# Kernel tuning notes

Hardware: AMD Instinct MI355X
Metric: run time of the kernel (lower is better)

The kernel has to match this reference:

```python
import math
import jax, jax.numpy as jnp
import numpy as np

B, S, D_IN, D_OUT = 8, 4096, 512, 512
CHUNK = 64
MAX_LR = 0.2        # config.max_memory_lr
MIN_DECAY = 0.5     # config.min_memory_decay
MAX_NORM = 30.0     # config.memory_max_norm
NORM_EPS = 1e-5     # config.norm_eps (used in normalize_for_delta)


def setup_inputs() -> dict:
    key = jax.random.key(0)
    ks = jax.random.split(key, 5)
    x = jax.random.normal(ks[0], (B, S, D_IN), dtype=jnp.float32)
    # M_init: xavier_uniform(gain=0.1) ~ small; use small normal
    M_init = jax.random.normal(ks[1], (D_OUT, D_IN), dtype=jnp.float32) * 0.02
    # hyperparam projections (Linear(d_in, 1)); torch init: zero weight, logit bias.
    # Use small random weights so the data-dependent path is exercised.
    eta_w = jax.random.normal(ks[2], (1, D_IN), dtype=jnp.float32) * 0.01
    eta_b = jnp.full((1,), math.log(0.08 / 0.92), dtype=jnp.float32)   # inv_sig(memory_lr_init)
    alpha_w = jax.random.normal(ks[3], (1, D_IN), dtype=jnp.float32) * 0.01
    alpha_b = jnp.full((1,), math.log(0.85 / 0.15), dtype=jnp.float32)  # inv_sig(memory_decay_init)
    gate_w = jax.random.normal(ks[4], (1, D_IN), dtype=jnp.float32) * 0.01
    gate_b = jnp.full((1,), 2.0, dtype=jnp.float32)
    return {"x": x, "M_init": M_init, "eta_w": eta_w, "eta_b": eta_b,
            "alpha_w": alpha_w, "alpha_b": alpha_b, "gate_w": gate_w, "gate_b": gate_b}


def _forward(x, M_init, eta_w, eta_b, alpha_w, alpha_b, gate_w, gate_b):
    n_chunks = S // CHUNK
    # [n_chunks, B, C, d_in] for scan over chunks
    xc = x.reshape(B, n_chunks, CHUNK, D_IN).transpose(1, 0, 2, 3)
    M0 = jnp.broadcast_to(M_init, (B, D_OUT, D_IN))

    def step(M, chunk):  # M: [B, d_out, d_in], chunk: [B, C, d_in]
        # per-chunk hyperparams (training mode: base logits = 0)
        eta_tok = jax.nn.sigmoid(chunk @ eta_w.T + eta_b) * MAX_LR            # [B,C,1]
        alpha_tok = MIN_DECAY + jax.nn.sigmoid(chunk @ alpha_w.T + alpha_b) * (1.0 - MIN_DECAY)
        eta = eta_tok.mean(axis=1, keepdims=True)    # [B,1,1]
        alpha = alpha_tok.mean(axis=1, keepdims=True)
        # retrieval: chunk @ M^T
        outputs = jnp.einsum('bcd,bod->bco', chunk, M)  # [B,C,d_out]
        # normalized keys (F.normalize: x / max(||x||, eps))
        kn = jnp.linalg.norm(chunk, axis=-1, keepdims=True)
        keys = chunk / jnp.maximum(kn, NORM_EPS)
        k_mean = keys.mean(axis=1)        # [B,d_in]
        v_target = outputs.mean(axis=1)   # [B,d_out]
        # delta rule rank-1 update
        Mk = jnp.einsum('bod,bd->bo', M, k_mean)
        error = v_target - Mk
        update = error[:, :, None] * k_mean[:, None, :]  # [B,d_out,d_in]
        # chunk_scale = min(C/chunk_size, 1) = 1 here
        M_new = alpha * M + eta * update
        gate = jax.nn.sigmoid(k_mean @ gate_w.T + gate_b)[:, :, None]  # [B,1,1]
        M_new = gate * M_new + (1.0 - gate) * M
        # frobenius-norm clamp
        M_norm = jnp.sqrt(jnp.sum(M_new * M_new, axis=(-2, -1), keepdims=True))
        scale = jnp.minimum(MAX_NORM / (M_norm + 1e-6), 1.0)
        return M_new * scale, outputs

    M_fin, outs = jax.lax.scan(step, M0, xc)  # outs: [n_chunks,B,C,d_out]
    out = outs.transpose(1, 0, 2, 3).reshape(B, S, D_OUT)
    return out, M_fin


def reference(x, M_init, eta_w, eta_b, alpha_w, alpha_b, gate_w, gate_b):
    return _forward(x, M_init, eta_w, eta_b, alpha_w, alpha_b, gate_w, gate_b)
```

## Files before the change

### kernel.cpp

```cpp
#include <hip/hip_runtime.h>
#include <math.h>

#define DIN  512
#define DOUT 512
#define CHK  64
#define NCH  64
#define NB   8
#define SEQ  4096

typedef short bh8_t __attribute__((ext_vector_type(8)));
typedef float f32x4 __attribute__((ext_vector_type(4)));

__device__ __forceinline__ float sigmoidf_(float z){ return 1.0f/(1.0f+__expf(-z)); }

__device__ __forceinline__ unsigned short f2bf(float f){
  unsigned u = __float_as_uint(f);
  unsigned r = (u + 0x7fffu + ((u>>16)&1u)) >> 16;
  return (unsigned short)r;
}
__device__ __forceinline__ void store_bf4(unsigned short* p, float4 v){
  uint2 u;
  u.x = (unsigned)f2bf(v.x) | ((unsigned)f2bf(v.y)<<16);
  u.y = (unsigned)f2bf(v.z) | ((unsigned)f2bf(v.w)<<16);
  *(uint2*)p = u;
}

__global__ __launch_bounds__(256) void k0_m0h(const float* __restrict__ M0, unsigned short* __restrict__ M0h){
  int idx = (blockIdx.x*256 + threadIdx.x)*4;
  float4 v = *(const float4*)(M0+idx);
  store_bf4(M0h+idx, v);
}

__global__ __launch_bounds__(256) void k1_stats(
    const float* __restrict__ x,
    const float* __restrict__ eta_w, const float* __restrict__ eta_b,
    const float* __restrict__ alpha_w, const float* __restrict__ alpha_b,
    const float* __restrict__ gate_w, const float* __restrict__ gate_b,
    float* __restrict__ KM, float* __restrict__ Dv, unsigned short* __restrict__ KMh,
    float* __restrict__ C1, float* __restrict__ C2, float* __restrict__ KM2, float* __restrict__ Q,
    unsigned short* __restrict__ xh)
{
  int j = blockIdx.x, b = blockIdx.y;
  const float* xc = x + ((size_t)b*SEQ + (size_t)j*CHK) * DIN;
  int tid = threadIdx.x;
  int wave = tid >> 6, lane = tid & 63;

  float km_acc[8], xb_acc[8];
#pragma unroll
  for (int k=0;k<8;k++){ km_acc[k]=0.f; xb_acc[k]=0.f; }
  float eta_sum = 0.f, alpha_sum = 0.f;
  float ew[8], aw[8];
#pragma unroll
  for (int k=0;k<8;k++){ ew[k]=eta_w[lane*8+k]; aw[k]=alpha_w[lane*8+k]; }

  for (int tt=0; tt<16; tt++){
    int t = wave*16 + tt;
    const float* xr = xc + (size_t)t*DIN + lane*8;
    float v[8];
#pragma unroll
    for (int k=0;k<8;k++) v[k]=xr[k];
    if (xh){
      uint4 hv;
      hv.x = (unsigned)f2bf(v[0]) | ((unsigned)f2bf(v[1])<<16);
      hv.y = (unsigned)f2bf(v[2]) | ((unsigned)f2bf(v[3])<<16);
      hv.z = (unsigned)f2bf(v[4]) | ((unsigned)f2bf(v[5])<<16);
      hv.w = (unsigned)f2bf(v[6]) | ((unsigned)f2bf(v[7])<<16);
      *(uint4*)&xh[((size_t)b*SEQ + (size_t)j*CHK + t)*DIN + lane*8] = hv;
    }
    float pe=0.f, pa=0.f, pn=0.f;
#pragma unroll
    for (int k=0;k<8;k++){ pe += v[k]*ew[k]; pa += v[k]*aw[k]; pn += v[k]*v[k]; }
#pragma unroll
    for (int off=32; off; off>>=1){
      pe += __shfl_xor(pe, off);
      pa += __shfl_xor(pa, off);
      pn += __shfl_xor(pn, off);
    }
    float inv = 1.0f / fmaxf(sqrtf(pn), 1e-5f);
    eta_sum   += sigmoidf_(pe + eta_b[0]);
    alpha_sum += sigmoidf_(pa + alpha_b[0]);
#pragma unroll
    for (int k=0;k<8;k++){ km_acc[k] += v[k]*inv; xb_acc[k] += v[k]; }
  }

  __shared__ float sKM[4][DIN];
  __shared__ float sXB[4][DIN];
  __shared__ float sEA[4][2];
  __shared__ float sred[4][2];
#pragma unroll
  for (int k=0;k<8;k++){ sKM[wave][lane*8+k]=km_acc[k]; sXB[wave][lane*8+k]=xb_acc[k]; }
  if (lane==0){ sEA[wave][0]=eta_sum; sEA[wave][1]=alpha_sum; }
  __syncthreads();

  float gpart=0.f, km2part=0.f;
  float kmv[2], dvv[2];
#pragma unroll
  for (int k=0;k<2;k++){
    int d = tid*2+k;
    float km = (sKM[0][d]+sKM[1][d]+sKM[2][d]+sKM[3][d]) * (1.0f/64.0f);
    float xb = (sXB[0][d]+sXB[1][d]+sXB[2][d]+sXB[3][d]) * (1.0f/64.0f);
    kmv[k]=km; dvv[k]=xb-km;
    gpart  += km * gate_w[d];
    km2part+= km * km;
  }
#pragma unroll
  for (int off=32; off; off>>=1){
    gpart   += __shfl_xor(gpart, off);
    km2part += __shfl_xor(km2part, off);
  }
  if (lane==0){ sred[wave][0]=gpart; sred[wave][1]=km2part; }
  __syncthreads();

  size_t base = ((size_t)b*NCH + j)*DIN;
#pragma unroll
  for (int k=0;k<2;k++){
    int d = tid*2+k;
    KM[base+d]=kmv[k];
    Dv[base+d]=dvv[k];
    KMh[base+d]=f2bf(kmv[k]);
  }
  if (tid==0){
    float gdot = sred[0][0]+sred[1][0]+sred[2][0]+sred[3][0];
    float km2  = sred[0][1]+sred[1][1]+sred[2][1]+sred[3][1];
    float etam = (sEA[0][0]+sEA[1][0]+sEA[2][0]+sEA[3][0]) * (1.0f/64.0f);
    float alpm = (sEA[0][1]+sEA[1][1]+sEA[2][1]+sEA[3][1]) * (1.0f/64.0f);
    float eta   = 0.2f * etam;
    float alpha = 0.5f + 0.5f * alpm;
    float gate  = sigmoidf_(gdot + gate_b[0]);
    float c1 = gate*alpha + 1.0f - gate;
    float c2 = gate*eta;
    C1[b*NCH+j]  = c1;
    C2[b*NCH+j]  = c2;
    KM2[b*NCH+j] = km2;
    Q[b*NCH+j]   = c2/c1;
  }
}

__global__ __launch_bounds__(256) void k2_g0h0(
    const float* __restrict__ KM, const float* __restrict__ Dv,
    const float* __restrict__ M0, float* __restrict__ G0, float* __restrict__ H0)
{
  int j = blockIdx.x, b = blockIdx.y, half = blockIdx.z;
  __shared__ float sD[DIN], sK[DIN];
  int tid = threadIdx.x;
  size_t base = ((size_t)b*NCH+j)*DIN;
  for (int d=tid; d<DIN; d+=256){ sD[d]=Dv[base+d]; sK[d]=KM[base+d]; }
  __syncthreads();
  int o = half*256 + tid;
  const float* mr = M0 + (size_t)o*DIN;
  float ag=0.f, ah=0.f;
  for (int d=0; d<DIN; d+=4){
    float4 m = *(const float4*)(mr+d);
    ag += m.x*sD[d] + m.y*sD[d+1] + m.z*sD[d+2] + m.w*sD[d+3];
    ah += m.x*sK[d] + m.y*sK[d+1] + m.z*sK[d+2] + m.w*sK[d+3];
  }
  G0[base+o]=ag; H0[base+o]=ah;
}

__global__ __launch_bounds__(512) void k2b_gram(
    const float* __restrict__ KM, const float* __restrict__ Dv,
    const float* __restrict__ Q,
    float* __restrict__ GT, float* __restrict__ WT)
{
  int i = blockIdx.x, b = blockIdx.y;
  __shared__ float sKi[DIN];
  int tid = threadIdx.x;
  const float* kmi = KM + ((size_t)b*NCH+i)*DIN;
  for (int d=tid; d<DIN; d+=512) sKi[d]=kmi[d];
  __syncthreads();
  float qi = Q[b*NCH+i];
  int wave = tid>>6, lane = tid&63;
  for (int j=wave; j<NCH; j+=8){
    const float* dj = Dv + ((size_t)b*NCH+j)*DIN;
    const float* kj = KM + ((size_t)b*NCH+j)*DIN;
    float pd=0.f, pk=0.f;
#pragma unroll
    for (int k=0;k<8;k++){
      int d = lane + k*64;
      pd += sKi[d]*dj[d];
      pk += sKi[d]*kj[d];
    }
#pragma unroll
    for (int off=32; off; off>>=1){ pd += __shfl_xor(pd,off); pk += __shfl_xor(pk,off); }
    if (lane==0){
      GT[((size_t)b*NCH+j)*NCH + i] = qi*pd;
      WT[((size_t)b*NCH+j)*NCH + i] = qi*pk;
    }
  }
}

__global__ __launch_bounds__(64) void k3a_rec(
    const float* __restrict__ G0, const float* __restrict__ H0,
    const float* __restrict__ GT, const float* __restrict__ WT,
    const float* __restrict__ Q,
    float* __restrict__ AU, unsigned short* __restrict__ UQTh, float* __restrict__ DOTS)
{
  int dblk = blockIdx.x, b = blockIdx.y;
  int lane = threadIdx.x;
  int d = dblk*64 + lane;

  __shared__ float sMT[NCH*NCH];
  __shared__ float sWT[NCH*NCH];
  __shared__ float sq[NCH];

  const float4* gt4 = (const float4*)&GT[(size_t)b*NCH*NCH];
  const float4* wt4 = (const float4*)&WT[(size_t)b*NCH*NCH];
#pragma unroll
  for (int t=0;t<16;t++){
    int idx4 = t*64 + lane;
    int idx  = idx4*4;
    int j = idx>>6, i0 = idx&63;
    float4 g = gt4[idx4];
    float4 w = wt4[idx4];
    if (i0+0 >= j){ g.x=0.f; w.x=0.f; }
    if (i0+1 >= j){ g.y=0.f; w.y=0.f; }
    if (i0+2 >= j){ g.z=0.f; w.z=0.f; }
    if (i0+3 >= j){ g.w=0.f; w.w=0.f; }
    *(float4*)&sMT[idx] = g;
    *(float4*)&sWT[idx] = w;
  }
  sq[lane] = Q[b*NCH+lane];
  __syncthreads();

  float au[NCH];
  size_t gb = (size_t)b*NCH*DOUT + d;
#pragma unroll
  for (int j=0;j<NCH;j++) au[j] = G0[gb + (size_t)j*DOUT];

#pragma unroll
  for (int j=1;j<NCH;j++){
    float a = au[j];
    const f32x4* row = (const f32x4*)&sMT[j*64];
    int ng = (j+3)>>2;
#pragma unroll
    for (int g=0; g<ng; g++){
      f32x4 c = row[g];
      a += c[0]*au[g*4+0] + c[1]*au[g*4+1] + c[2]*au[g*4+2] + c[3]*au[g*4+3];
    }
    au[j] = a;
  }
#pragma unroll
  for (int j=0;j<NCH;j++) AU[gb + (size_t)j*DOUT] = au[j];

#pragma unroll
  for (int g=0; g<8; g++){
    uint4 hv;
    hv.x = (unsigned)f2bf(au[g*8+0]*sq[g*8+0]) | ((unsigned)f2bf(au[g*8+1]*sq[g*8+1])<<16);
    hv.y = (unsigned)f2bf(au[g*8+2]*sq[g*8+2]) | ((unsigned)f2bf(au[g*8+3]*sq[g*8+3])<<16);
    hv.z = (unsigned)f2bf(au[g*8+4]*sq[g*8+4]) | ((unsigned)f2bf(au[g*8+5]*sq[g*8+5])<<16);
    hv.w = (unsigned)f2bf(au[g*8+6]*sq[g*8+6]) | ((unsigned)f2bf(au[g*8+7]*sq[g*8+7])<<16);
    *(uint4*)&UQTh[((size_t)b*DOUT + d)*NCH + g*8] = hv;
  }

#pragma unroll
  for (int j=0;j<NCH;j++){
    float w = H0[gb + (size_t)j*DOUT];
    const f32x4* row = (const f32x4*)&sWT[j*64];
    int ng = (j+3)>>2;
#pragma unroll
    for (int g=0; g<ng; g++){
      f32x4 c = row[g];
      w += c[0]*au[g*4+0] + c[1]*au[g*4+1] + c[2]*au[g*4+2] + c[3]*au[g*4+3];
    }
    float s1 = au[j]*w, s2 = au[j]*au[j];
#pragma unroll
    for (int off=32; off; off>>=1){ s1+=__shfl_xor(s1,off); s2+=__shfl_xor(s2,off); }
    if (lane==0){
      DOTS[(((size_t)b*8+dblk)*NCH+j)*2+0] = s1;
      DOTS[(((size_t)b*8+dblk)*NCH+j)*2+1] = s2;
    }
  }
}

__global__ __launch_bounds__(256) void k3b_chain(
    const float* __restrict__ M0, const float* __restrict__ DOTS,
    const float* __restrict__ C1, const float* __restrict__ C2, const float* __restrict__ KM2,
    float* __restrict__ P)
{
  int b = blockIdx.x;
  int tid = threadIdx.x, wave = tid>>6, lane = tid&63;
  __shared__ float sF[4];
  __shared__ float suw[NCH], suu[NCH], sc1[NCH], sc2[NCH], skm2[NCH];

  float f0p = 0.f;
  const float4* m4 = (const float4*)M0;
  for (int i=tid; i<(DOUT*DIN)/4; i+=256){
    float4 v = m4[i];
    f0p += v.x*v.x + v.y*v.y + v.z*v.z + v.w*v.w;
  }
#pragma unroll
  for (int off=32; off; off>>=1) f0p += __shfl_xor(f0p, off);
  if (lane==0) sF[wave]=f0p;

  if (tid < NCH){
    float uw=0.f, uu=0.f;
#pragma unroll
    for (int k=0;k<8;k++){
      uw += DOTS[(((size_t)b*8+k)*NCH+tid)*2+0];
      uu += DOTS[(((size_t)b*8+k)*NCH+tid)*2+1];
    }
    suw[tid]=uw; suu[tid]=uu;
    sc1[tid]=C1[b*NCH+tid]; sc2[tid]=C2[b*NCH+tid]; skm2[tid]=KM2[b*NCH+tid];
  }
  __syncthreads();

  if (tid==0){
    float F = sF[0]+sF[1]+sF[2]+sF[3];
    float p = 1.f;
    P[b*65+0] = 1.f;
    for (int j=0;j<NCH;j++){
      float uw = suw[j], uu = suu[j];
      float c1 = sc1[j], c2 = sc2[j], km2 = skm2[j];
      uw *= p*p; uu *= p*p;
      float Fnew = c1*c1*F + 2.f*c1*c2*uw + c2*c2*uu*km2;
      float scale = fminf(30.0f/(sqrtf(Fnew)+1e-6f), 1.0f);
      F = scale*scale*Fnew;
      p = scale*c1*p;
      P[b*65+j+1] = p;
    }
  }
}

__global__ __launch_bounds__(256) void k4s_s(
    const float* __restrict__ x, const unsigned short* __restrict__ xh,
    const unsigned short* __restrict__ KMh,
    unsigned short* __restrict__ Sh, int use_xh)
{
  int tt = blockIdx.x, b = blockIdx.y;
  int tid = threadIdx.x;
  int lane = tid&63, w = tid>>6, m = lane&15, q = lane>>4;
  __shared__ unsigned short As[64*72];
  __shared__ unsigned short Bs[64*72];
  f32x4 acc[4];
  f32x4 z = {0.f,0.f,0.f,0.f};
#pragma unroll
  for (int nf=0;nf<4;nf++) acc[nf]=z;

  for (int k0=0;k0<DIN;k0+=64){
    uint4 bb[2];
#pragma unroll
    for (int v=0;v<2;v++){
      int idx=v*256+tid; int il=idx>>3, cc=idx&7;
      bb[v] = *(const uint4*)&KMh[((size_t)b*NCH+il)*DIN + k0 + cc*8];
    }
    if (use_xh){
      uint4 av[2];
#pragma unroll
      for (int v=0;v<2;v++){
        int idx=v*256+tid; int row=idx>>3, cc=idx&7;
        av[v] = *(const uint4*)&xh[((size_t)b*SEQ + (size_t)tt*64 + row)*DIN + k0 + cc*8];
      }
      __syncthreads();
#pragma unroll
      for (int v=0;v<2;v++){
        int idx=v*256+tid; int row=idx>>3, cc=idx&7;
        *(uint4*)&As[row*72 + cc*8] = av[v];
      }
    } else {
      float4 xa[4];
#pragma unroll
      for (int v=0;v<4;v++){
        int idx=v*256+tid; int row=idx>>4, cc=idx&15;
        xa[v] = *(const float4*)(x + ((size_t)b*SEQ + (size_t)tt*64 + row)*DIN + k0 + cc*4);
      }
      __syncthreads();
#pragma unroll
      for (int v=0;v<4;v++){
        int idx=v*256+tid; int row=idx>>4, cc=idx&15;
        store_bf4(&As[row*72 + cc*4], xa[v]);
      }
    }
#pragma unroll
    for (int v=0;v<2;v++){
      int idx=v*256+tid; int il=idx>>3, cc=idx&7;
      *(uint4*)&Bs[il*72 + cc*8] = bb[v];
    }
    __syncthreads();
#pragma unroll
    for (int kk=0;kk<2;kk++){
      bh8_t af = *(bh8_t*)&As[(w*16+m)*72 + kk*32 + q*8];
#pragma unroll
      for (int nf=0;nf<4;nf++){
        bh8_t bf_ = *(bh8_t*)&Bs[(nf*16+m)*72 + kk*32 + q*8];
        acc[nf] = __builtin_amdgcn_mfma_f32_16x16x32_bf16(af, bf_, acc[nf], 0,0,0);
      }
    }
  }
  __syncthreads();
  unsigned short* tb = As + w*16*72;
#pragma unroll
  for (int nf=0;nf<4;nf++)
#pragma unroll
    for (int r=0;r<4;r++)
      tb[(q*4+r)*72 + nf*16 + m] = f2bf(acc[nf][r]);
#pragma unroll
  for (int v=0;v<2;v++){
    int idx = v*64 + lane;
    int row = idx>>3, c8 = idx&7;
    uint4 vv = *(uint4*)&tb[row*72 + c8*8];
    *(uint4*)&Sh[((size_t)b*SEQ + (size_t)tt*64 + w*16 + row)*NCH + c8*8] = vv;
  }
}

__global__ __launch_bounds__(512, 4) void k4_out(
    const float* __restrict__ x, const unsigned short* __restrict__ xh,
    const unsigned short* __restrict__ M0h,
    const unsigned short* __restrict__ Sh, const unsigned short* __restrict__ UQTh,
    const float* __restrict__ P, float* __restrict__ out, int use_xh)
{
  int ot = blockIdx.x, rb = blockIdx.y, b = blockIdx.z;
  int tid = threadIdx.x;
  int lane = tid&63, w = tid>>6, m = lane&15, q = lane>>4;
  int wr = w>>1, wc = w&1;
  int O0 = ot*128;
  int R0 = rb*256;

  __shared__ __align__(16) char pool[55296];
  unsigned short* As = (unsigned short*)pool;
  unsigned short* Bs = (unsigned short*)pool + 256*72;
  float* ep = (float*)pool;

  f32x4 acc[4][4];
  f32x4 z = {0.f,0.f,0.f,0.f};
#pragma unroll
  for (int mi=0;mi<4;mi++)
#pragma unroll
    for (int nf=0;nf<4;nf++) acc[mi][nf]=z;

#pragma unroll
  for (int v=0; v<4; v++){
    int idx = v*512 + tid;
    int row = idx>>3, cc = idx&7;
    int j = (R0 + row)>>6;
    uint4 sv = *(const uint4*)&Sh[((size_t)b*SEQ + R0 + row)*NCH + cc*8];
    int i0 = cc*8;
    unsigned m0 = (i0+0 < j) ? ((i0+1 < j)?0xFFFFFFFFu:0x0000FFFFu) : 0u;
    unsigned m1 = (i0+2 < j) ? ((i0+3 < j)?0xFFFFFFFFu:0x0000FFFFu) : 0u;
    unsigned m2 = (i0+4 < j) ? ((i0+5 < j)?0xFFFFFFFFu:0x0000FFFFu) : 0u;
    unsigned m3 = (i0+6 < j) ? ((i0+7 < j)?0xFFFFFFFFu:0x0000FFFFu) : 0u;
    sv.x&=m0; sv.y&=m1; sv.z&=m2; sv.w&=m3;
    *(uint4*)&As[row*72 + cc*8] = sv;
  }
#pragma unroll
  for (int v=0; v<2; v++){
    int idx = v*512 + tid;
    int ol = idx>>3, cc = idx&7;
    *(uint4*)&Bs[ol*72 + cc*8] = *(const uint4*)&UQTh[((size_t)b*DOUT + O0+ol)*NCH + cc*8];
  }
  __syncthreads();
#pragma unroll
  for (int kk=0;kk<2;kk++){
#pragma unroll
    for (int mi=0;mi<4;mi++){
      bh8_t af = *(bh8_t*)&As[(wr*64+mi*16+m)*72 + kk*32 + q*8];
#pragma unroll
      for (int nf=0;nf<4;nf++){
        bh8_t bf_ = *(bh8_t*)&Bs[(wc*64+nf*16+m)*72 + kk*32 + q*8];
        acc[mi][nf] = __builtin_amdgcn_mfma_f32_16x16x32_bf16(af, bf_, acc[mi][nf], 0,0,0);
      }
    }
  }

  for (int k0=0;k0<DIN;k0+=64){
    uint4 bb[2];
#pragma unroll
    for (int v=0;v<2;v++){
      int idx=v*512+tid; int ol=idx>>3, cc=idx&7;
      bb[v] = *(const uint4*)&M0h[(size_t)(O0+ol)*DIN + k0 + cc*8];
    }
    if (use_xh){
      uint4 av[4];
#pragma unroll
      for (int v=0;v<4;v++){
        int idx=v*512+tid; int row=idx>>3, cc=idx&7;
        av[v] = *(const uint4*)&xh[((size_t)b*SEQ + R0 + row)*DIN + k0 + cc*8];
      }
      __syncthreads();
#pragma unroll
      for (int v=0;v<4;v++){
        int idx=v*512+tid; int row=idx>>3, cc=idx&7;
        *(uint4*)&As[row*72 + cc*8] = av[v];
      }
    } else {
      float4 xa[8];
#pragma unroll
      for (int v=0;v<8;v++){
        int idx=v*512+tid; int row=idx>>4, cc=idx&15;
        xa[v] = *(const float4*)(x + ((size_t)b*SEQ + R0 + row)*DIN + k0 + cc*4);
      }
      __syncthreads();
#pragma unroll
      for (int v=0;v<8;v++){
        int idx=v*512+tid; int row=idx>>4, cc=idx&15;
        store_bf4(&As[row*72 + cc*4], xa[v]);
      }
    }
#pragma unroll
    for (int v=0;v<2;v++){
      int idx=v*512+tid; int ol=idx>>3, cc=idx&7;
      *(uint4*)&Bs[ol*72 + cc*8] = bb[v];
    }
    __syncthreads();
#pragma unroll
    for (int kk=0;kk<2;kk++){
#pragma unroll
      for (int mi=0;mi<4;mi++){
        bh8_t af = *(bh8_t*)&As[(wr*64+mi*16+m)*72 + kk*32 + q*8];
#pragma unroll
        for (int nf=0;nf<4;nf++){
          bh8_t bf_ = *(bh8_t*)&Bs[(wc*64+nf*16+m)*72 + kk*32 + q*8];
          acc[mi][nf] = __builtin_amdgcn_mfma_f32_16x16x32_bf16(af, bf_, acc[mi][nf], 0,0,0);
        }
      }
    }
  }

  __syncthreads();
  float p = P[b*65 + rb*4 + wr];
  float* epw = ep + w*(16*68);
#pragma unroll
  for (int mi=0; mi<4; mi++){
#pragma unroll
    for (int nf=0;nf<4;nf++)
#pragma unroll
      for (int r=0;r<4;r++)
        epw[(q*4+r)*68 + nf*16 + m] = p*acc[mi][nf][r];
#pragma unroll
    for (int v=0;v<4;v++){
      int idx = v*64 + lane;
      int row = idx>>4, c4 = idx&15;
      float4 vv = *(float4*)&epw[row*68 + c4*4];
      *(float4*)&out[((size_t)b*SEQ + R0 + wr*64 + mi*16 + row)*DOUT + O0 + wc*64 + c4*4] = vv;
    }
  }
}

__global__ __launch_bounds__(256) void k5_mfin(
    const float* __restrict__ M0, const float* __restrict__ KM,
    const float* __restrict__ AU, const float* __restrict__ P, const float* __restrict__ Q,
    float* __restrict__ Mout)
{
  int ob = blockIdx.x, b = blockIdx.y;
  int tid = threadIdx.x;
  __shared__ float uo[64][8];
  for (int idx=tid; idx<512; idx+=256){
    int i = idx>>3, oo = idx&7;
    uo[i][oo] = Q[b*NCH+i] * AU[((size_t)b*NCH+i)*DOUT + ob*8+oo];
  }
  __syncthreads();
  float p64 = P[b*65+NCH];
  float acc[2][8];
#pragma unroll
  for (int h=0;h<2;h++)
#pragma unroll
    for (int oo=0;oo<8;oo++) acc[h][oo]=0.f;
  int d0 = tid, d1 = tid+256;
  for (int i=0;i<64;i++){
    float k0 = KM[((size_t)b*NCH+i)*DIN + d0];
    float k1 = KM[((size_t)b*NCH+i)*DIN + d1];
#pragma unroll
    for (int oo=0;oo<8;oo++){
      float u = uo[i][oo];
      acc[0][oo] += u*k0;
      acc[1][oo] += u*k1;
    }
  }
#pragma unroll
  for (int oo=0;oo<8;oo++){
    int o = ob*8+oo;
    Mout[((size_t)b*DOUT + o)*DIN + d0] = p64*(M0[(size_t)o*DIN+d0] + acc[0][oo]);
    Mout[((size_t)b*DOUT + o)*DIN + d1] = p64*(M0[(size_t)o*DIN+d1] + acc[1][oo]);
  }
}

extern "C" void kernel_launch(void* const* d_in, const int* in_sizes, int n_in,
                              void* d_out, int out_size, void* d_ws, size_t ws_size,
                              hipStream_t stream) {
  const float* x       = (const float*)d_in[0];
  const float* M0      = (const float*)d_in[1];
  const float* eta_w   = (const float*)d_in[2];
  const float* eta_b   = (const float*)d_in[3];
  const float* alpha_w = (const float*)d_in[4];
  const float* alpha_b = (const float*)d_in[5];
  const float* gate_w  = (const float*)d_in[6];
  const float* gate_b  = (const float*)d_in[7];
  float* out = (float*)d_out;

  float* ws = (float*)d_ws;
  float* KM   = ws;
  float* Dv   = KM   + 262144;
  float* G0   = Dv   + 262144;
  float* H0   = G0   + 262144;
  float* AU   = H0   + 262144;
  float* GT   = AU   + 262144;
  float* WT   = GT   + 32768;
  float* C1   = WT   + 32768;
  float* C2   = C1   + 512;
  float* KM2  = C2   + 512;
  float* Q    = KM2  + 512;
  float* P    = Q    + 512;
  float* DOTS = P    + 1024;
  unsigned short* M0h  = (unsigned short*)(DOTS + 8192);
  unsigned short* KMh  = M0h  + 262144;
  unsigned short* Sh   = KMh  + 262144;
  unsigned short* UQTh = Sh   + 2097152;
  unsigned short* xh   = UQTh + 262144;

  size_t base_bytes = (size_t)((char*)xh - (char*)d_ws);
  size_t need_xh = base_bytes + (size_t)16777216*2;
  int use_xh = (ws_size >= need_xh) ? 1 : 0;
  unsigned short* xh_arg = use_xh ? xh : (unsigned short*)0;

  k0_m0h<<<dim3(256), 256, 0, stream>>>(M0, M0h);
  k1_stats<<<dim3(NCH, NB), 256, 0, stream>>>(x, eta_w, eta_b, alpha_w, alpha_b,
                                              gate_w, gate_b, KM, Dv, KMh, C1, C2, KM2, Q, xh_arg);
  k2_g0h0<<<dim3(NCH, NB, 2), 256, 0, stream>>>(KM, Dv, M0, G0, H0);
  k2b_gram<<<dim3(NCH, NB), 512, 0, stream>>>(KM, Dv, Q, GT, WT);
  k4s_s<<<dim3(SEQ/64, NB), 256, 0, stream>>>(x, xh, KMh, Sh, use_xh);
  k3a_rec<<<dim3(8, NB), 64, 0, stream>>>(G0, H0, GT, WT, Q, AU, UQTh, DOTS);
  k3b_chain<<<dim3(NB), 256, 0, stream>>>(M0, DOTS, C1, C2, KM2, P);
  k4_out<<<dim3(4, SEQ/256, NB), 512, 0, stream>>>(x, xh, M0h, Sh, UQTh, P, out, use_xh);
  k5_mfin<<<dim3(64, NB), 256, 0, stream>>>(M0, KM, AU, P, Q, out + (size_t)NB*SEQ*DOUT);
}
```

Before: 480.6 us.

## Prefetch next K-tile into registers, remap blocks per XCD, widen LDS stride in k4_out

```diff
diff --git a/kernel.cpp b/kernel.cpp
--- a/kernel.cpp
+++ b/kernel.cpp
@@ -402,22 +402,27 @@
   }
 }
 
+#define ASTRIDE 80
 __global__ __launch_bounds__(512, 4) void k4_out(
     const float* __restrict__ x, const unsigned short* __restrict__ xh,
     const unsigned short* __restrict__ M0h,
     const unsigned short* __restrict__ Sh, const unsigned short* __restrict__ UQTh,
     const float* __restrict__ P, float* __restrict__ out, int use_xh)
 {
-  int ot = blockIdx.x, rb = blockIdx.y, b = blockIdx.z;
+  int n = blockIdx.x;
+  int xcd = n & 7, local = n >> 3;
+  int work = xcd*64 + local;
+  int ot = work & 3, rb = (work>>2) & 15, b = work >> 6;
+
   int tid = threadIdx.x;
   int lane = tid&63, w = tid>>6, m = lane&15, q = lane>>4;
   int wr = w>>1, wc = w&1;
   int O0 = ot*128;
   int R0 = rb*256;
 
-  __shared__ __align__(16) char pool[55296];
+  __shared__ __align__(16) char pool[(256+128)*ASTRIDE*2];
   unsigned short* As = (unsigned short*)pool;
-  unsigned short* Bs = (unsigned short*)pool + 256*72;
+  unsigned short* Bs = (unsigned short*)pool + 256*ASTRIDE;
   float* ep = (float*)pool;
 
   f32x4 acc[4][4];
@@ -439,76 +444,100 @@
     unsigned m2 = (i0+4 < j) ? ((i0+5 < j)?0xFFFFFFFFu:0x0000FFFFu) : 0u;
     unsigned m3 = (i0+6 < j) ? ((i0+7 < j)?0xFFFFFFFFu:0x0000FFFFu) : 0u;
     sv.x&=m0; sv.y&=m1; sv.z&=m2; sv.w&=m3;
-    *(uint4*)&As[row*72 + cc*8] = sv;
+    *(uint4*)&As[row*ASTRIDE + cc*8] = sv;
   }
 #pragma unroll
   for (int v=0; v<2; v++){
     int idx = v*512 + tid;
     int ol = idx>>3, cc = idx&7;
-    *(uint4*)&Bs[ol*72 + cc*8] = *(const uint4*)&UQTh[((size_t)b*DOUT + O0+ol)*NCH + cc*8];
-  }
+    *(uint4*)&Bs[ol*ASTRIDE + cc*8] = *(const uint4*)&UQTh[((size_t)b*DOUT + O0+ol)*NCH + cc*8];
+  }
+
+  uint4 pB[2], pA[4];
+  float4 xa[8];
+#pragma unroll
+  for (int v=0;v<2;v++){
+    int idx=v*512+tid; int ol=idx>>3, cc=idx&7;
+    pB[v] = *(const uint4*)&M0h[(size_t)(O0+ol)*DIN + 0 + cc*8];
+  }
+  if (use_xh){
+#pragma unroll
+    for (int v=0;v<4;v++){
+      int idx=v*512+tid; int row=idx>>3, cc=idx&7;
+      pA[v] = *(const uint4*)&xh[((size_t)b*SEQ + R0 + row)*DIN + 0 + cc*8];
+    }
+  } else {
+#pragma unroll
+    for (int v=0;v<8;v++){
+      int idx=v*512+tid; int row=idx>>4, cc=idx&15;
+      xa[v] = *(const float4*)(x + ((size_t)b*SEQ + R0 + row)*DIN + 0 + cc*4);
+    }
+  }
+
   __syncthreads();
 #pragma unroll
   for (int kk=0;kk<2;kk++){
 #pragma unroll
     for (int mi=0;mi<4;mi++){
-      bh8_t af = *(bh8_t*)&As[(wr*64+mi*16+m)*72 + kk*32 + q*8];
+      bh8_t af = *(bh8_t*)&As[(wr*64+mi*16+m)*ASTRIDE + kk*32 + q*8];
 #pragma unroll
       for (int nf=0;nf<4;nf++){
-        bh8_t bf_ = *(bh8_t*)&Bs[(wc*64+nf*16+m)*72 + kk*32 + q*8];
+        bh8_t bf_ = *(bh8_t*)&Bs[(wc*64+nf*16+m)*ASTRIDE + kk*32 + q*8];
         acc[mi][nf] = __builtin_amdgcn_mfma_f32_16x16x32_bf16(af, bf_, acc[mi][nf], 0,0,0);
       }
     }
   }
 
   for (int k0=0;k0<DIN;k0+=64){
-    uint4 bb[2];
+    __syncthreads();
 #pragma unroll
     for (int v=0;v<2;v++){
       int idx=v*512+tid; int ol=idx>>3, cc=idx&7;
-      bb[v] = *(const uint4*)&M0h[(size_t)(O0+ol)*DIN + k0 + cc*8];
+      *(uint4*)&Bs[ol*ASTRIDE + cc*8] = pB[v];
     }
     if (use_xh){
-      uint4 av[4];
 #pragma unroll
       for (int v=0;v<4;v++){
         int idx=v*512+tid; int row=idx>>3, cc=idx&7;
-        av[v] = *(const uint4*)&xh[((size_t)b*SEQ + R0 + row)*DIN + k0 + cc*8];
-      }
-      __syncthreads();
-#pragma unroll
-      for (int v=0;v<4;v++){
-        int idx=v*512+tid; int row=idx>>3, cc=idx&7;
-        *(uint4*)&As[row*72 + cc*8] = av[v];
+        *(uint4*)&As[row*ASTRIDE + cc*8] = pA[v];
       }
     } else {
-      float4 xa[8];
 #pragma unroll
       for (int v=0;v<8;v++){
         int idx=v*512+tid; int row=idx>>4, cc=idx&15;
-        xa[v] = *(const float4*)(x + ((size_t)b*SEQ + R0 + row)*DIN + k0 + cc*4);
-      }
-      __syncthreads();
-#pragma unroll
-      for (int v=0;v<8;v++){
-        int idx=v*512+tid; int row=idx>>4, cc=idx&15;
-        store_bf4(&As[row*72 + cc*4], xa[v]);
-      }
-    }
-#pragma unroll
-    for (int v=0;v<2;v++){
-      int idx=v*512+tid; int ol=idx>>3, cc=idx&7;
-      *(uint4*)&Bs[ol*72 + cc*8] = bb[v];
+        store_bf4(&As[row*ASTRIDE + cc*4], xa[v]);
+      }
+    }
+    int kn = k0 + 64;
+    if (kn < DIN){
+#pragma unroll
+      for (int v=0;v<2;v++){
+        int idx=v*512+tid; int ol=idx>>3, cc=idx&7;
+        pB[v] = *(const uint4*)&M0h[(size_t)(O0+ol)*DIN + kn + cc*8];
+      }
+      if (use_xh){
+#pragma unroll
+        for (int v=0;v<4;v++){
+          int idx=v*512+tid; int row=idx>>3, cc=idx&7;
+          pA[v] = *(const uint4*)&xh[((size_t)b*SEQ + R0 + row)*DIN + kn + cc*8];
+        }
+      } else {
+#pragma unroll
+        for (int v=0;v<8;v++){
+          int idx=v*512+tid; int row=idx>>4, cc=idx&15;
+          xa[v] = *(const float4*)(x + ((size_t)b*SEQ + R0 + row)*DIN + kn + cc*4);
+        }
+      }
     }
     __syncthreads();
 #pragma unroll
     for (int kk=0;kk<2;kk++){
 #pragma unroll
       for (int mi=0;mi<4;mi++){
-        bh8_t af = *(bh8_t*)&As[(wr*64+mi*16+m)*72 + kk*32 + q*8];
+        bh8_t af = *(bh8_t*)&As[(wr*64+mi*16+m)*ASTRIDE + kk*32 + q*8];
 #pragma unroll
         for (int nf=0;nf<4;nf++){
-          bh8_t bf_ = *(bh8_t*)&Bs[(wc*64+nf*16+m)*72 + kk*32 + q*8];
+          bh8_t bf_ = *(bh8_t*)&Bs[(wc*64+nf*16+m)*ASTRIDE + kk*32 + q*8];
           acc[mi][nf] = __builtin_amdgcn_mfma_f32_16x16x32_bf16(af, bf_, acc[mi][nf], 0,0,0);
         }
       }
@@ -619,6 +648,6 @@
   k4s_s<<<dim3(SEQ/64, NB), 256, 0, stream>>>(x, xh, KMh, Sh, use_xh);
   k3a_rec<<<dim3(8, NB), 64, 0, stream>>>(G0, H0, GT, WT, Q, AU, UQTh, DOTS);
   k3b_chain<<<dim3(NB), 256, 0, stream>>>(M0, DOTS, C1, C2, KM2, P);
-  k4_out<<<dim3(4, SEQ/256, NB), 512, 0, stream>>>(x, xh, M0h, Sh, UQTh, P, out, use_xh);
+  k4_out<<<dim3(512), 512, 0, stream>>>(x, xh, M0h, Sh, UQTh, P, out, use_xh);
   k5_mfin<<<dim3(64, NB), 256, 0, stream>>>(M0, KM, AU, P, Q, out + (size_t)NB*SEQ*DOUT);
 }
```

New measurement: 476.9 us. No clear change (-0.8%).
